# Performance work log

Measured on AMD Instinct MI355X. Metric: run time of the kernel, lower is better.

The kernel has to match this reference:

```python
import jax, jax.numpy as jnp
import numpy as np

D_MODEL = 1024
N_HEADS = 16


def setup_inputs() -> dict:
    key = jax.random.key(0)
    ks = jax.random.split(key, 5)
    B, T, C = 4, 2048, D_MODEL
    x = jax.random.normal(ks[0], (B, T, C), dtype=jnp.float32)
    W_attn = jax.random.normal(ks[1], (C, 3 * C), dtype=jnp.float32) * (1.0 / np.sqrt(C))
    b_attn = jnp.zeros((3 * C,), dtype=jnp.float32)
    W_proj = jax.random.normal(ks[2], (C, C), dtype=jnp.float32) * (1.0 / np.sqrt(C))
    b_proj = jnp.zeros((C,), dtype=jnp.float32)
    return {"x": x, "W_attn": W_attn, "b_attn": b_attn, "W_proj": W_proj, "b_proj": b_proj}


def reference(x, W_attn, b_attn, W_proj, b_proj):
    B, T, C = x.shape
    H = N_HEADS
    hd = C // H
    qkv = x @ W_attn + b_attn                      # [B,T,3C]
    q, k, v = jnp.split(qkv, 3, axis=2)
    # [B,T,C] -> [B,H,T,hd]
    q = q.reshape(B, T, H, hd).transpose(0, 2, 1, 3)
    k = k.reshape(B, T, H, hd).transpose(0, 2, 1, 3)
    v = v.reshape(B, T, H, hd).transpose(0, 2, 1, 3)
    scale = 1.0 / jnp.sqrt(jnp.float32(hd))
    attn = jnp.einsum('bhqd,bhkd->bhqk', q, k) * scale
    causal = jnp.tril(jnp.ones((T, T), dtype=bool))
    attn = jnp.where(causal[None, None], attn, -jnp.inf)
    w = jax.nn.softmax(attn, axis=-1)
    ctx = jnp.einsum('bhqk,bhkd->bhqd', w, v)      # [B,H,T,hd]
    ctx = ctx.transpose(0, 2, 1, 3).reshape(B, T, C)
    return ctx @ W_proj + b_proj
```

## Files before the change

kernel.cpp:

```cpp
#include <hip/hip_runtime.h>
#include <hip/hip_bf16.h>

typedef __bf16 bf16x8 __attribute__((ext_vector_type(8)));
typedef __bf16 bf16x4 __attribute__((ext_vector_type(4)));
typedef float f32x4 __attribute__((ext_vector_type(4)));

#define MFMA(A, B, C) __builtin_amdgcn_mfma_f32_16x16x32_bf16((A), (B), (C), 0, 0, 0)

#if __has_builtin(__builtin_amdgcn_exp2f)
#define EXP2(x) __builtin_amdgcn_exp2f(x)
#else
#define EXP2(x) exp2f(x)
#endif

#define T_SEQ 2048
#define BATCH 4
#define CDIM  1024
#define HEADS 16
#define HD    64
#define MROWS (BATCH * T_SEQ)
#define QK_SCALE 0.18033688011112042f
#define KTILES (CDIM / 64)

__device__ __forceinline__ void async_ld16(const __bf16* g, __bf16* l) {
    __builtin_amdgcn_global_load_lds(
        (const __attribute__((address_space(1))) void*)g,
        (__attribute__((address_space(3))) void*)l, 16, 0, 0);
}

__global__ __launch_bounds__(256) void conv_transpose(const float* __restrict__ src,
                                                      __bf16* __restrict__ dst,
                                                      int R, int C)
{
    __shared__ float tile[32][33];
    int c0 = blockIdx.x * 32, r0 = blockIdx.y * 32;
    int tx = threadIdx.x, ty = threadIdx.y;
#pragma unroll
    for (int i = 0; i < 4; i++)
        tile[ty + i * 8][tx] = src[(long)(r0 + ty + i * 8) * C + c0 + tx];
    __syncthreads();
#pragma unroll
    for (int i = 0; i < 4; i++)
        dst[(long)(c0 + ty + i * 8) * R + r0 + tx] = (__bf16)tile[tx][ty + i * 8];
}

__global__ __launch_bounds__(256) void conv_bf16(const float* __restrict__ src,
                                                 __bf16* __restrict__ dst)
{
    long i = ((long)blockIdx.x * 256 + threadIdx.x) * 8;
    f32x4 f0 = ((const f32x4*)(src + i))[0];
    f32x4 f1 = ((const f32x4*)(src + i))[1];
    bf16x8 v;
#pragma unroll
    for (int j = 0; j < 4; j++) { v[j] = (__bf16)f0[j]; v[4 + j] = (__bf16)f1[j]; }
    *(bf16x8*)(dst + i) = v;
}

__global__ __launch_bounds__(256) void vtrans(const __bf16* __restrict__ qkv,
                                              __bf16* __restrict__ vt)
{
    __shared__ __bf16 tile[32][33];
    int bh = blockIdx.z;
    int b = bh >> 4, h = bh & 15;
    int t0 = blockIdx.x * 32, d0 = blockIdx.y * 32;
    int tx = threadIdx.x, ty = threadIdx.y;
#pragma unroll
    for (int i = 0; i < 4; i++)
        tile[ty + i * 8][tx] =
            qkv[(long)(b * T_SEQ + t0 + ty + i * 8) * (3 * CDIM) + 2 * CDIM + h * HD + d0 + tx];
    __syncthreads();
#pragma unroll
    for (int i = 0; i < 4; i++)
        vt[(long)(bh * HD + d0 + ty + i * 8) * T_SEQ + t0 + tx] = tile[tx][ty + i * 8];
}


#define QS_ALO(p, kt)                                                            \
    do {                                                                         \
        async_ld16(Asrc + (long)(kt) * 64, &Ab[p][sdst]);                        \
        async_ld16(Asrc + (long)128 * CDIM + (kt) * 64, &Ab[p][8192 + sdst]);    \
    } while (0)
#define QS_AHI(p, kt)                                                            \
    do {                                                                         \
        async_ld16(Asrc + (long)64 * CDIM + (kt) * 64, &Ab[p][4096 + sdst]);     \
        async_ld16(Asrc + (long)192 * CDIM + (kt) * 64, &Ab[p][12288 + sdst]);   \
    } while (0)
#define QS_B(p, kt)                                                              \
    do {                                                                         \
        async_ld16(Bsrc + (long)(kt) * 64, &Bb[p][sdst]);                        \
        async_ld16(Bsrc + (long)64 * CDIM + (kt) * 64, &Bb[p][4096 + sdst]);     \
        async_ld16(Bsrc + (long)128 * CDIM + (kt) * 64, &Bb[p][8192 + sdst]);    \
    } while (0)

__global__ __launch_bounds__(512, 2) void gemm_qkv(const __bf16* __restrict__ A,
                                                   const __bf16* __restrict__ Bt,
                                                   const float* __restrict__ bias,
                                                   __bf16* __restrict__ C)
{
    __shared__ __attribute__((aligned(16))) __bf16 Ab[2][256 * 64];
    __shared__ __attribute__((aligned(16))) __bf16 Bb[2][192 * 64];

    const int bid = (int)blockIdx.x;
    const int swz = (bid & 7) * 64 + (bid >> 3);
    const int n0 = (swz & 15) * 192;
    const int m0 = (swz >> 4) * 256;

    const int t = threadIdx.x;
    const int wave = t >> 6, lane = t & 63;
    const int quad = lane >> 4, l15 = lane & 15;
    const int wm = wave >> 2, wn = wave & 3;

    const int srow = t >> 3;
    const int scol = ((t & 7) * 8) ^ ((srow & 7) << 3);
    const int sdst = srow * 64 + (t & 7) * 8;
    const __bf16* Asrc = A + (long)(m0 + srow) * CDIM + scol;
    const __bf16* Bsrc = Bt + (long)(n0 + srow) * CDIM + scol;

    const int kx0 = (quad * 8) ^ ((l15 & 7) << 3);
    const int kx1 = (32 + quad * 8) ^ ((l15 & 7) << 3);
    const int aro = (wm * 128 + l15) * 64;
    const int bro = (wn * 48 + l15) * 64;

    f32x4 acc[8][3] = {};
    bf16x8 A0[4][2], A1[4][2], B0[2][2], B1[2];

    QS_ALO(0, 0); QS_AHI(0, 0); QS_B(0, 0);
    QS_ALO(1, 1); QS_AHI(1, 1); QS_B(1, 1);
    asm volatile("s_waitcnt vmcnt(7)" ::: "memory");
    __builtin_amdgcn_s_barrier();
#pragma unroll
    for (int mf = 0; mf < 4; mf++) {
        A0[mf][0] = *(const bf16x8*)&Ab[0][aro + mf * 1024 + kx0];
        A0[mf][1] = *(const bf16x8*)&Ab[0][aro + mf * 1024 + kx1];
    }
#pragma unroll
    for (int nf = 0; nf < 2; nf++) {
        B0[nf][0] = *(const bf16x8*)&Bb[0][bro + nf * 1024 + kx0];
        B0[nf][1] = *(const bf16x8*)&Bb[0][bro + nf * 1024 + kx1];
    }

#pragma unroll 2
    for (int kt = 0; kt < KTILES; ++kt) {
        const int cur = kt & 1, nxt = cur ^ 1;

#pragma unroll
        for (int mf = 0; mf < 4; mf++) {
            A1[mf][0] = *(const bf16x8*)&Ab[cur][aro + 4096 + mf * 1024 + kx0];
            A1[mf][1] = *(const bf16x8*)&Ab[cur][aro + 4096 + mf * 1024 + kx1];
        }
        __builtin_amdgcn_s_barrier();
        asm volatile("s_waitcnt lgkmcnt(8)");
        __builtin_amdgcn_sched_barrier(0);
        __builtin_amdgcn_s_setprio(1);
#pragma unroll
        for (int mf = 0; mf < 4; mf++)
#pragma unroll
            for (int nf = 0; nf < 2; nf++) {
                acc[mf][nf] = MFMA(A0[mf][0], B0[nf][0], acc[mf][nf]);
                acc[mf][nf] = MFMA(A0[mf][1], B0[nf][1], acc[mf][nf]);
            }
        __builtin_amdgcn_s_setprio(0);
        __builtin_amdgcn_s_barrier();

        B1[0] = *(const bf16x8*)&Bb[cur][bro + 2048 + kx0];
        B1[1] = *(const bf16x8*)&Bb[cur][bro + 2048 + kx1];
        if (kt + 2 < KTILES) QS_ALO(cur, kt + 2);
        __builtin_amdgcn_s_barrier();
        asm volatile("s_waitcnt lgkmcnt(2)");
        __builtin_amdgcn_sched_barrier(0);
        __builtin_amdgcn_s_setprio(1);
#pragma unroll
        for (int mf = 0; mf < 4; mf++)
#pragma unroll
            for (int nf = 0; nf < 2; nf++) {
                acc[4 + mf][nf] = MFMA(A1[mf][0], B0[nf][0], acc[4 + mf][nf]);
                acc[4 + mf][nf] = MFMA(A1[mf][1], B0[nf][1], acc[4 + mf][nf]);
            }
        __builtin_amdgcn_s_setprio(0);
        if (kt + 2 < KTILES) { asm volatile("s_waitcnt vmcnt(2)" ::: "memory"); }
        else                 { asm volatile("s_waitcnt vmcnt(0)" ::: "memory"); }
        __builtin_amdgcn_s_barrier();

        if (kt + 2 < KTILES) QS_AHI(cur, kt + 2);
        if (kt + 1 < KTILES) {
#pragma unroll
            for (int nf = 0; nf < 2; nf++) {
                B0[nf][0] = *(const bf16x8*)&Bb[nxt][bro + nf * 1024 + kx0];
                B0[nf][1] = *(const bf16x8*)&Bb[nxt][bro + nf * 1024 + kx1];
            }
        }
        __builtin_amdgcn_s_barrier();
        asm volatile("s_waitcnt lgkmcnt(4)");
        __builtin_amdgcn_sched_barrier(0);
        __builtin_amdgcn_s_setprio(1);
#pragma unroll
        for (int mf = 0; mf < 4; mf++) {
            acc[mf][2] = MFMA(A0[mf][0], B1[0], acc[mf][2]);
            acc[mf][2] = MFMA(A0[mf][1], B1[1], acc[mf][2]);
        }
        __builtin_amdgcn_s_setprio(0);
        __builtin_amdgcn_s_barrier();

        if (kt + 2 < KTILES) QS_B(cur, kt + 2);
        if (kt + 1 < KTILES) {
#pragma unroll
            for (int mf = 0; mf < 4; mf++) {
                A0[mf][0] = *(const bf16x8*)&Ab[nxt][aro + mf * 1024 + kx0];
                A0[mf][1] = *(const bf16x8*)&Ab[nxt][aro + mf * 1024 + kx1];
            }
        }
        __builtin_amdgcn_s_barrier();
        asm volatile("s_waitcnt lgkmcnt(8)");
        __builtin_amdgcn_sched_barrier(0);
        __builtin_amdgcn_s_setprio(1);
#pragma unroll
        for (int mf = 0; mf < 4; mf++) {
            acc[4 + mf][2] = MFMA(A1[mf][0], B1[0], acc[4 + mf][2]);
            acc[4 + mf][2] = MFMA(A1[mf][1], B1[1], acc[4 + mf][2]);
        }
        __builtin_amdgcn_s_setprio(0);
        __builtin_amdgcn_s_barrier();
    }

#pragma unroll
    for (int mf = 0; mf < 8; mf++) {
#pragma unroll
        for (int nf = 0; nf < 3; nf++) {
            const int col = n0 + wn * 48 + nf * 16 + l15;
            const float bv = bias[col];
            const float sc = (col < CDIM) ? QK_SCALE : 1.0f;
#pragma unroll
            for (int r = 0; r < 4; r++) {
                const int row = m0 + wm * 128 + (mf >> 2) * 64 + (mf & 3) * 16 + quad * 4 + r;
                C[(long)row * (3 * CDIM) + col] = (__bf16)((acc[mf][nf][r] + bv) * sc);
            }
        }
    }
}

#define PS_A(p, kt)                                                              \
    do {                                                                         \
        async_ld16(Asrc + (long)(kt) * 64, &Ab[p][sdst]);                        \
        async_ld16(Asrc + (long)64 * (3 * CDIM) + (kt) * 64, &Ab[p][4096 + sdst]); \
    } while (0)
#define PS_B(p, kt)                                                              \
    do {                                                                         \
        async_ld16(Bsrc + (long)(kt) * 64, &Bb[p][sdst]);                        \
        async_ld16(Bsrc + (long)64 * CDIM + (kt) * 64, &Bb[p][4096 + sdst]);     \
        async_ld16(Bsrc + (long)128 * CDIM + (kt) * 64, &Bb[p][8192 + sdst]);    \
        async_ld16(Bsrc + (long)192 * CDIM + (kt) * 64, &Bb[p][12288 + sdst]);   \
    } while (0)

__global__ __launch_bounds__(512, 2) void gemm_proj(const __bf16* __restrict__ A,
                                                    const __bf16* __restrict__ Bt,
                                                    const float* __restrict__ bias,
                                                    float* __restrict__ C)
{
    __shared__ __attribute__((aligned(16))) __bf16 Ab[2][128 * 64];
    __shared__ __attribute__((aligned(16))) __bf16 Bb[2][256 * 64];

    const int bid = (int)blockIdx.x;
    const int swz = (bid & 7) * 32 + (bid >> 3);
    const int n0 = (swz & 3) * 256;
    const int m0 = (swz >> 2) * 128;

    const int t = threadIdx.x;
    const int wave = t >> 6, lane = t & 63;
    const int quad = lane >> 4, l15 = lane & 15;
    const int wm = wave >> 2, wn = wave & 3;

    const int srow = t >> 3;
    const int scol = ((t & 7) * 8) ^ ((srow & 7) << 3);
    const int sdst = srow * 64 + (t & 7) * 8;
    const __bf16* Asrc = A + (long)(m0 + srow) * (3 * CDIM) + scol;
    const __bf16* Bsrc = Bt + (long)(n0 + srow) * CDIM + scol;

    const int kx0 = (quad * 8) ^ ((l15 & 7) << 3);
    const int kx1 = (32 + quad * 8) ^ ((l15 & 7) << 3);
    const int aro = (wm * 64 + l15) * 64;
    const int bro = (wn * 64 + l15) * 64;

    f32x4 acc[4][4] = {};
    bf16x8 A0[2][2], A1[2][2], B0[2][2], B1[2][2];

    PS_A(0, 0); PS_B(0, 0);
    PS_A(1, 1); PS_B(1, 1);
    asm volatile("s_waitcnt vmcnt(6)" ::: "memory");
    __builtin_amdgcn_s_barrier();
#pragma unroll
    for (int mf = 0; mf < 2; mf++) {
        A0[mf][0] = *(const bf16x8*)&Ab[0][aro + mf * 1024 + kx0];
        A0[mf][1] = *(const bf16x8*)&Ab[0][aro + mf * 1024 + kx1];
    }
#pragma unroll
    for (int nf = 0; nf < 2; nf++) {
        B0[nf][0] = *(const bf16x8*)&Bb[0][bro + nf * 1024 + kx0];
        B0[nf][1] = *(const bf16x8*)&Bb[0][bro + nf * 1024 + kx1];
    }

#pragma unroll 2
    for (int kt = 0; kt < KTILES; ++kt) {
        const int cur = kt & 1, nxt = cur ^ 1;

#pragma unroll
        for (int mf = 0; mf < 2; mf++) {
            A1[mf][0] = *(const bf16x8*)&Ab[cur][aro + 2048 + mf * 1024 + kx0];
            A1[mf][1] = *(const bf16x8*)&Ab[cur][aro + 2048 + mf * 1024 + kx1];
        }
        __builtin_amdgcn_s_barrier();
        asm volatile("s_waitcnt lgkmcnt(4)");
        __builtin_amdgcn_sched_barrier(0);
        __builtin_amdgcn_s_setprio(1);
#pragma unroll
        for (int mf = 0; mf < 2; mf++)
#pragma unroll
            for (int nf = 0; nf < 2; nf++) {
                acc[mf][nf] = MFMA(A0[mf][0], B0[nf][0], acc[mf][nf]);
                acc[mf][nf] = MFMA(A0[mf][1], B0[nf][1], acc[mf][nf]);
            }
        __builtin_amdgcn_s_setprio(0);
        __builtin_amdgcn_s_barrier();

#pragma unroll
        for (int nf = 0; nf < 2; nf++) {
            B1[nf][0] = *(const bf16x8*)&Bb[cur][bro + 2048 + nf * 1024 + kx0];
            B1[nf][1] = *(const bf16x8*)&Bb[cur][bro + 2048 + nf * 1024 + kx1];
        }
        __builtin_amdgcn_s_barrier();
        asm volatile("s_waitcnt lgkmcnt(4)");
        __builtin_amdgcn_sched_barrier(0);
        __builtin_amdgcn_s_setprio(1);
#pragma unroll
        for (int mf = 0; mf < 2; mf++)
#pragma unroll
            for (int nf = 0; nf < 2; nf++) {
                acc[2 + mf][nf] = MFMA(A1[mf][0], B0[nf][0], acc[2 + mf][nf]);
                acc[2 + mf][nf] = MFMA(A1[mf][1], B0[nf][1], acc[2 + mf][nf]);
            }
        __builtin_amdgcn_s_setprio(0);
        asm volatile("s_waitcnt vmcnt(0)" ::: "memory");
        __builtin_amdgcn_s_barrier();

        if (kt + 2 < KTILES) PS_A(cur, kt + 2);
        if (kt + 1 < KTILES) {
#pragma unroll
            for (int nf = 0; nf < 2; nf++) {
                B0[nf][0] = *(const bf16x8*)&Bb[nxt][bro + nf * 1024 + kx0];
                B0[nf][1] = *(const bf16x8*)&Bb[nxt][bro + nf * 1024 + kx1];
            }
        }
        __builtin_amdgcn_s_barrier();
        asm volatile("s_waitcnt lgkmcnt(4)");
        __builtin_amdgcn_sched_barrier(0);
        __builtin_amdgcn_s_setprio(1);
#pragma unroll
        for (int mf = 0; mf < 2; mf++)
#pragma unroll
            for (int nf = 0; nf < 2; nf++) {
                acc[mf][2 + nf] = MFMA(A0[mf][0], B1[nf][0], acc[mf][2 + nf]);
                acc[mf][2 + nf] = MFMA(A0[mf][1], B1[nf][1], acc[mf][2 + nf]);
            }
        __builtin_amdgcn_s_setprio(0);
        __builtin_amdgcn_s_barrier();

        if (kt + 2 < KTILES) PS_B(cur, kt + 2);
        if (kt + 1 < KTILES) {
#pragma unroll
            for (int mf = 0; mf < 2; mf++) {
                A0[mf][0] = *(const bf16x8*)&Ab[nxt][aro + mf * 1024 + kx0];
                A0[mf][1] = *(const bf16x8*)&Ab[nxt][aro + mf * 1024 + kx1];
            }
        }
        __builtin_amdgcn_s_barrier();
        asm volatile("s_waitcnt lgkmcnt(4)");
        __builtin_amdgcn_sched_barrier(0);
        __builtin_amdgcn_s_setprio(1);
#pragma unroll
        for (int mf = 0; mf < 2; mf++)
#pragma unroll
            for (int nf = 0; nf < 2; nf++) {
                acc[2 + mf][2 + nf] = MFMA(A1[mf][0], B1[nf][0], acc[2 + mf][2 + nf]);
                acc[2 + mf][2 + nf] = MFMA(A1[mf][1], B1[nf][1], acc[2 + mf][2 + nf]);
            }
        __builtin_amdgcn_s_setprio(0);
        __builtin_amdgcn_s_barrier();
    }

#pragma unroll
    for (int mf = 0; mf < 4; mf++) {
#pragma unroll
        for (int nf = 0; nf < 4; nf++) {
            const int col = n0 + wn * 64 + (nf >> 1) * 32 + (nf & 1) * 16 + l15;
            const float bv = bias[col];
#pragma unroll
            for (int r = 0; r < 4; r++) {
                const int row = m0 + wm * 64 + (mf >> 1) * 32 + (mf & 1) * 16 + quad * 4 + r;
                C[(long)row * CDIM + col] = acc[mf][nf][r] + bv;
            }
        }
    }
}

#define ATT_STAGE(p, kt_)                                                        \
    do {                                                                         \
        const __bf16* kp_ = kglob + (long)(kt_) * 64 * (3 * CDIM);               \
        async_ld16(kp_, &Ks[p][t * 8]);                                          \
        async_ld16(kp_ + (long)32 * (3 * CDIM), &Ks[p][t * 8 + 2048]);           \
        const __bf16* vp_ = vglob + (kt_) * 64;                                  \
        async_ld16(vp_, &Vts[p][t * 8]);                                         \
        async_ld16(vp_ + (long)32 * T_SEQ, &Vts[p][t * 8 + 2048]);               \
    } while (0)

__global__ __launch_bounds__(256) void attn_kernel(__bf16* qkv,
                                                   const __bf16* __restrict__ vt)
{
    __shared__ __attribute__((aligned(16))) __bf16 Ks[2][64 * 64];
    __shared__ __attribute__((aligned(16))) __bf16 Vts[2][64 * 64];
    __shared__ __attribute__((aligned(16))) __bf16 Ps[8][16 * 64];

    const int bh = blockIdx.x;
    const int b = bh >> 4, h = bh & 15;
    const int qt = (int)gridDim.y - 1 - (int)blockIdx.y;
    const int q0 = qt * 128;
    const int t = threadIdx.x;
    const int wave = t >> 6, lane = t & 63;
    const int quad = lane >> 4, l15 = lane & 15;

    const int srow = t >> 3;
    const int scol = (((t & 7) ^ (srow & 7)) << 3);
    const __bf16* kglob = qkv + (long)(b * T_SEQ + srow) * (3 * CDIM) + CDIM + h * HD + scol;
    const __bf16* vglob = vt + ((long)bh * HD + srow) * T_SEQ + scol;

    const int kx0 = (quad * 8) ^ ((l15 & 7) << 3);
    const int kx1 = (32 + quad * 8) ^ ((l15 & 7) << 3);

    bf16x8 qfr[2][2];
#pragma unroll
    for (int f = 0; f < 2; f++) {
        const __bf16* qb = qkv + (long)(b * T_SEQ + q0 + f * 64 + wave * 16 + l15) * (3 * CDIM) + h * HD;
        qfr[f][0] = *(const bf16x8*)(qb + quad * 8);
        qfr[f][1] = *(const bf16x8*)(qb + 32 + quad * 8);
    }

    bf16x8 vone;
#pragma unroll
    for (int j = 0; j < 8; j++) vone[j] = (__bf16)1.0f;

    f32x4 Oacc[2][4] = {};
    f32x4 lacc[2] = {};

    const int qb0 = q0 + wave * 16;
    const int ntiles = (q0 + 128) / 64;

    ATT_STAGE(0, 0);
    for (int kt = 0; kt < ntiles; kt++) {
        const int cur = kt & 1;
        const int kv0 = kt * 64;
        if (kt + 1 < ntiles) {
            ATT_STAGE(cur ^ 1, kt + 1);
            asm volatile("s_waitcnt vmcnt(4)" ::: "memory");
        } else {
            asm volatile("s_waitcnt vmcnt(0)" ::: "memory");
        }
        __builtin_amdgcn_s_barrier();
        asm volatile("" ::: "memory");

#pragma unroll
        for (int c = 0; c < 4; c++) {
            const int rk = c * 16 + l15;
            bf16x8 kf0 = *(const bf16x8*)&Ks[cur][rk * 64 + kx0];
            bf16x8 kf1 = *(const bf16x8*)&Ks[cur][rk * 64 + kx1];
#pragma unroll
            for (int f = 0; f < 2; f++) {
                const int qbf = qb0 + f * 64;
                if (kv0 > qbf + 15) continue;
                __bf16* pdst = &Ps[wave * 2 + f][l15 * 64 +
                                ((((c * 2 + (quad >> 1)) ^ (l15 & 7)) << 3) + (quad & 1) * 4)];
                if (kv0 + c * 16 > qbf + 15) {
                    bf16x4 zz = {};
                    *(bf16x4*)pdst = zz;
                    continue;
                }
                f32x4 z = {};
                z = MFMA(kf0, qfr[f][0], z);
                z = MFMA(kf1, qfr[f][1], z);
                bf16x4 pk;
                if (kv0 + 63 > qbf) {
                    const int qg = qbf + l15;
                    const int kvb = kv0 + c * 16 + quad * 4;
#pragma unroll
                    for (int r = 0; r < 4; r++) {
                        float v = (kvb + r > qg) ? -1e30f : z[r];
                        pk[r] = (__bf16)EXP2(v);
                    }
                } else {
#pragma unroll
                    for (int r = 0; r < 4; r++)
                        pk[r] = (__bf16)EXP2(z[r]);
                }
                *(bf16x4*)pdst = pk;
            }
        }

        __threadfence_block();

        const bool act0 = (kv0 <= qb0 + 15);
        bf16x8 pf[2][2];
#pragma unroll
        for (int f = 0; f < 2; f++) {
            if (f == 0 && !act0) continue;
            pf[f][0] = *(const bf16x8*)&Ps[wave * 2 + f][l15 * 64 + kx0];
            pf[f][1] = *(const bf16x8*)&Ps[wave * 2 + f][l15 * 64 + kx1];
            lacc[f] = MFMA(pf[f][0], vone, lacc[f]);
            lacc[f] = MFMA(pf[f][1], vone, lacc[f]);
        }
#pragma unroll
        for (int n = 0; n < 4; n++) {
            const int rv = n * 16 + l15;
            bf16x8 vf0 = *(const bf16x8*)&Vts[cur][rv * 64 + kx0];
            bf16x8 vf1 = *(const bf16x8*)&Vts[cur][rv * 64 + kx1];
            if (act0) {
                Oacc[0][n] = MFMA(pf[0][0], vf0, Oacc[0][n]);
                Oacc[0][n] = MFMA(pf[0][1], vf1, Oacc[0][n]);
            }
            Oacc[1][n] = MFMA(pf[1][0], vf0, Oacc[1][n]);
            Oacc[1][n] = MFMA(pf[1][1], vf1, Oacc[1][n]);
        }
        __builtin_amdgcn_s_barrier();
        asm volatile("" ::: "memory");
    }

#pragma unroll
    for (int f = 0; f < 2; f++)
#pragma unroll
        for (int n = 0; n < 4; n++) {
            int col = h * HD + n * 16 + l15;
#pragma unroll
            for (int r = 0; r < 4; r++) {
                int row = q0 + f * 64 + wave * 16 + quad * 4 + r;
                float val = Oacc[f][n][r] / lacc[f][r];
                qkv[(long)(b * T_SEQ + row) * (3 * CDIM) + col] = (__bf16)val;
            }
        }
}

extern "C" void kernel_launch(void* const* d_in, const int* in_sizes, int n_in,
                              void* d_out, int out_size, void* d_ws, size_t ws_size,
                              hipStream_t stream) {
    (void)in_sizes; (void)n_in; (void)out_size; (void)ws_size;
    const float* x  = (const float*)d_in[0];
    const float* Wa = (const float*)d_in[1];
    const float* ba = (const float*)d_in[2];
    const float* Wp = (const float*)d_in[3];
    const float* bp = (const float*)d_in[4];
    float* out = (float*)d_out;

    char* ws = (char*)d_ws;
    __bf16* qkv = (__bf16*)(ws);
    __bf16* Wat = (__bf16*)(ws + 50331648);
    __bf16* vt  = (__bf16*)(ws + 50331648);
    __bf16* Wpt = (__bf16*)(ws + 50331648);
    __bf16* xbf = (__bf16*)d_out;

    conv_bf16<<<dim3(MROWS * CDIM / (256 * 8)), 256, 0, stream>>>(x, xbf);
    conv_transpose<<<dim3(3 * CDIM / 32, CDIM / 32), dim3(32, 8), 0, stream>>>(Wa, Wat, CDIM, 3 * CDIM);

    gemm_qkv<<<dim3(512), 512, 0, stream>>>(xbf, Wat, ba, qkv);

    vtrans<<<dim3(T_SEQ / 32, HD / 32, BATCH * HEADS), dim3(32, 8), 0, stream>>>(qkv, vt);

    attn_kernel<<<dim3(BATCH * HEADS, T_SEQ / 128), 256, 0, stream>>>(qkv, vt);

    conv_transpose<<<dim3(CDIM / 32, CDIM / 32), dim3(32, 8), 0, stream>>>(Wp, Wpt, CDIM, CDIM);

    gemm_proj<<<dim3(256), 512, 0, stream>>>(qkv, Wpt, bp, out);
}
```

Baseline: 262.3 us.

## Replace async LDS K/V double buffer with register-prefetch single buffer in attention

The attention kernel stops using async global-to-LDS loads into a double-buffered 64x64 K/V tile. Each K/V tile is now prefetched into registers one step ahead and written into a single LDS buffer split into two 32-column halves, using a new XOR swizzle. The P staging buffer is padded to a 72-element row stride, and launch bounds request 4 blocks per SIMD. The aim is to cut LDS footprint and raise occupancy, at the cost of more barriers per tile and more register pressure from the prefetched values.

```diff
diff --git a/kernel.cpp b/kernel.cpp
--- a/kernel.cpp
+++ b/kernel.cpp
@@ -401,22 +401,30 @@
     }
 }
 
-#define ATT_STAGE(p, kt_)                                                        \
+#define ATT_LOAD(k0_, k1_, v0_, v1_, kt_)                                        \
     do {                                                                         \
         const __bf16* kp_ = kglob + (long)(kt_) * 64 * (3 * CDIM);               \
-        async_ld16(kp_, &Ks[p][t * 8]);                                          \
-        async_ld16(kp_ + (long)32 * (3 * CDIM), &Ks[p][t * 8 + 2048]);           \
+        k0_ = *(const bf16x8*)kp_;                                               \
+        k1_ = *(const bf16x8*)(kp_ + 32);                                        \
         const __bf16* vp_ = vglob + (kt_) * 64;                                  \
-        async_ld16(vp_, &Vts[p][t * 8]);                                         \
-        async_ld16(vp_ + (long)32 * T_SEQ, &Vts[p][t * 8 + 2048]);               \
-    } while (0)
-
-__global__ __launch_bounds__(256) void attn_kernel(__bf16* qkv,
-                                                   const __bf16* __restrict__ vt)
+        v0_ = *(const bf16x8*)vp_;                                               \
+        v1_ = *(const bf16x8*)(vp_ + 32);                                        \
+    } while (0)
+
+#define ATT_WRITE(k0_, k1_, v0_, v1_)                                            \
+    do {                                                                         \
+        *(bf16x8*)&Ks[0][wdst] = k0_;                                            \
+        *(bf16x8*)&Ks[1][wdst] = k1_;                                            \
+        *(bf16x8*)&Vts[0][wdst] = v0_;                                           \
+        *(bf16x8*)&Vts[1][wdst] = v1_;                                           \
+    } while (0)
+
+__global__ __launch_bounds__(256, 4) void attn_kernel(__bf16* qkv,
+                                                      const __bf16* __restrict__ vt)
 {
-    __shared__ __attribute__((aligned(16))) __bf16 Ks[2][64 * 64];
-    __shared__ __attribute__((aligned(16))) __bf16 Vts[2][64 * 64];
-    __shared__ __attribute__((aligned(16))) __bf16 Ps[8][16 * 64];
+    __shared__ __attribute__((aligned(16))) __bf16 Ks[2][64 * 32];
+    __shared__ __attribute__((aligned(16))) __bf16 Vts[2][64 * 32];
+    __shared__ __attribute__((aligned(16))) __bf16 Ps[8][16 * 72];
 
     const int bh = blockIdx.x;
     const int b = bh >> 4, h = bh & 15;
@@ -426,14 +434,6 @@
     const int wave = t >> 6, lane = t & 63;
     const int quad = lane >> 4, l15 = lane & 15;
 
-    const int srow = t >> 3;
-    const int scol = (((t & 7) ^ (srow & 7)) << 3);
-    const __bf16* kglob = qkv + (long)(b * T_SEQ + srow) * (3 * CDIM) + CDIM + h * HD + scol;
-    const __bf16* vglob = vt + ((long)bh * HD + srow) * T_SEQ + scol;
-
-    const int kx0 = (quad * 8) ^ ((l15 & 7) << 3);
-    const int kx1 = (32 + quad * 8) ^ ((l15 & 7) << 3);
-
     bf16x8 qfr[2][2];
 #pragma unroll
     for (int f = 0; f < 2; f++) {
@@ -449,85 +449,100 @@
     f32x4 Oacc[2][4] = {};
     f32x4 lacc[2] = {};
 
+    const __bf16* kglob = qkv + (long)(b * T_SEQ + (t >> 2)) * (3 * CDIM)
+                          + CDIM + h * HD + (t & 3) * 8;
+    const __bf16* vglob = vt + ((long)bh * HD + (t >> 2)) * T_SEQ + (t & 3) * 8;
+    const int wdst = (t >> 2) * 32 + (((t & 3) ^ ((t >> 3) & 3)) << 3);
+    const int qx8 = (quad ^ ((l15 >> 1) & 3)) << 3;
+
     const int qb0 = q0 + wave * 16;
     const int ntiles = (q0 + 128) / 64;
 
-    ATT_STAGE(0, 0);
-    for (int kt = 0; kt < ntiles; kt++) {
-        const int cur = kt & 1;
-        const int kv0 = kt * 64;
-        if (kt + 1 < ntiles) {
-            ATT_STAGE(cur ^ 1, kt + 1);
-            asm volatile("s_waitcnt vmcnt(4)" ::: "memory");
-        } else {
-            asm volatile("s_waitcnt vmcnt(0)" ::: "memory");
-        }
-        __builtin_amdgcn_s_barrier();
-        asm volatile("" ::: "memory");
-
-#pragma unroll
-        for (int c = 0; c < 4; c++) {
-            const int rk = c * 16 + l15;
-            bf16x8 kf0 = *(const bf16x8*)&Ks[cur][rk * 64 + kx0];
-            bf16x8 kf1 = *(const bf16x8*)&Ks[cur][rk * 64 + kx1];
+    bf16x8 kA0, kA1, vA0, vA1, kB0, kB1, vB0, vB1;
+    ATT_LOAD(kA0, kA1, vA0, vA1, 0);
+
+    for (int kt = 0; kt < ntiles; kt += 2) {
+        asm volatile("s_waitcnt lgkmcnt(0)" ::: "memory");
+        __builtin_amdgcn_s_barrier();
+        ATT_LOAD(kB0, kB1, vB0, vB1, kt + 1);
+        ATT_WRITE(kA0, kA1, vA0, vA1);
+        asm volatile("s_waitcnt lgkmcnt(0)" ::: "memory");
+        __builtin_amdgcn_s_barrier();
+
+#pragma unroll
+        for (int half = 0; half < 2; half++) {
+            const int kv0 = (kt + half) * 64;
+
+#pragma unroll
+            for (int c = 0; c < 4; c++) {
+                const int rk = c * 16 + l15;
+                bf16x8 kf0 = *(const bf16x8*)&Ks[0][rk * 32 + qx8];
+                bf16x8 kf1 = *(const bf16x8*)&Ks[1][rk * 32 + qx8];
+#pragma unroll
+                for (int f = 0; f < 2; f++) {
+                    const int qbf = qb0 + f * 64;
+                    if (kv0 > qbf + 15) continue;
+                    __bf16* pdst = &Ps[wave * 2 + f][l15 * 72 + c * 16 + quad * 4];
+                    if (kv0 + c * 16 > qbf + 15) {
+                        bf16x4 zz = {};
+                        *(bf16x4*)pdst = zz;
+                        continue;
+                    }
+                    f32x4 z = {};
+                    z = MFMA(kf0, qfr[f][0], z);
+                    z = MFMA(kf1, qfr[f][1], z);
+                    bf16x4 pk;
+                    if (kv0 + 63 > qbf) {
+                        const int qg = qbf + l15;
+                        const int kvb = kv0 + c * 16 + quad * 4;
+#pragma unroll
+                        for (int r = 0; r < 4; r++) {
+                            float v = (kvb + r > qg) ? -1e30f : z[r];
+                            pk[r] = (__bf16)EXP2(v);
+                        }
+                    } else {
+#pragma unroll
+                        for (int r = 0; r < 4; r++)
+                            pk[r] = (__bf16)EXP2(z[r]);
+                    }
+                    *(bf16x4*)pdst = pk;
+                }
+            }
+
+            __threadfence_block();
+
+            const bool act0 = (kv0 <= qb0 + 15);
+            bf16x8 pf[2][2];
 #pragma unroll
             for (int f = 0; f < 2; f++) {
-                const int qbf = qb0 + f * 64;
-                if (kv0 > qbf + 15) continue;
-                __bf16* pdst = &Ps[wave * 2 + f][l15 * 64 +
-                                ((((c * 2 + (quad >> 1)) ^ (l15 & 7)) << 3) + (quad & 1) * 4)];
-                if (kv0 + c * 16 > qbf + 15) {
-                    bf16x4 zz = {};
-                    *(bf16x4*)pdst = zz;
-                    continue;
+                if (f == 0 && !act0) continue;
+                pf[f][0] = *(const bf16x8*)&Ps[wave * 2 + f][l15 * 72 + quad * 8];
+                pf[f][1] = *(const bf16x8*)&Ps[wave * 2 + f][l15 * 72 + 32 + quad * 8];
+                lacc[f] = MFMA(pf[f][0], vone, lacc[f]);
+                lacc[f] = MFMA(pf[f][1], vone, lacc[f]);
+            }
+#pragma unroll
+            for (int n = 0; n < 4; n++) {
+                const int rv = n * 16 + l15;
+                bf16x8 vf0 = *(const bf16x8*)&Vts[0][rv * 32 + qx8];
+                bf16x8 vf1 = *(const bf16x8*)&Vts[1][rv * 32 + qx8];
+                if (act0) {
+                    Oacc[0][n] = MFMA(pf[0][0], vf0, Oacc[0][n]);
+                    Oacc[0][n] = MFMA(pf[0][1], vf1, Oacc[0][n]);
                 }
-                f32x4 z = {};
-                z = MFMA(kf0, qfr[f][0], z);
-                z = MFMA(kf1, qfr[f][1], z);
-                bf16x4 pk;
-                if (kv0 + 63 > qbf) {
-                    const int qg = qbf + l15;
-                    const int kvb = kv0 + c * 16 + quad * 4;
-#pragma unroll
-                    for (int r = 0; r < 4; r++) {
-                        float v = (kvb + r > qg) ? -1e30f : z[r];
-                        pk[r] = (__bf16)EXP2(v);
-                    }
-                } else {
-#pragma unroll
-                    for (int r = 0; r < 4; r++)
-                        pk[r] = (__bf16)EXP2(z[r]);
-                }
-                *(bf16x4*)pdst = pk;
-            }
-        }
-
-        __threadfence_block();
-
-        const bool act0 = (kv0 <= qb0 + 15);
-        bf16x8 pf[2][2];
-#pragma unroll
-        for (int f = 0; f < 2; f++) {
-            if (f == 0 && !act0) continue;
-            pf[f][0] = *(const bf16x8*)&Ps[wave * 2 + f][l15 * 64 + kx0];
-            pf[f][1] = *(const bf16x8*)&Ps[wave * 2 + f][l15 * 64 + kx1];
-            lacc[f] = MFMA(pf[f][0], vone, lacc[f]);
-            lacc[f] = MFMA(pf[f][1], vone, lacc[f]);
-        }
-#pragma unroll
-        for (int n = 0; n < 4; n++) {
-            const int rv = n * 16 + l15;
-            bf16x8 vf0 = *(const bf16x8*)&Vts[cur][rv * 64 + kx0];
-            bf16x8 vf1 = *(const bf16x8*)&Vts[cur][rv * 64 + kx1];
-            if (act0) {
-                Oacc[0][n] = MFMA(pf[0][0], vf0, Oacc[0][n]);
-                Oacc[0][n] = MFMA(pf[0][1], vf1, Oacc[0][n]);
-            }
-            Oacc[1][n] = MFMA(pf[1][0], vf0, Oacc[1][n]);
-            Oacc[1][n] = MFMA(pf[1][1], vf1, Oacc[1][n]);
-        }
-        __builtin_amdgcn_s_barrier();
-        asm volatile("" ::: "memory");
+                Oacc[1][n] = MFMA(pf[1][0], vf0, Oacc[1][n]);
+                Oacc[1][n] = MFMA(pf[1][1], vf1, Oacc[1][n]);
+            }
+
+            if (half == 0) {
+                asm volatile("s_waitcnt lgkmcnt(0)" ::: "memory");
+                __builtin_amdgcn_s_barrier();
+                if (kt + 2 < ntiles) ATT_LOAD(kA0, kA1, vA0, vA1, kt + 2);
+                ATT_WRITE(kB0, kB1, vB0, vB1);
+                asm volatile("s_waitcnt lgkmcnt(0)" ::: "memory");
+                __builtin_amdgcn_s_barrier();
+            }
+        }
     }
 
 #pragma unroll
```

After: 271.0 us. +3.3%, slower.
